# Optimization experiments

Measured on AMD Instinct MI355X. Metric: run time of the kernel, lower is better.

The kernel has to match this reference:

```python
import jax, jax.numpy as jnp
import numpy as np

T, D = 256, 256
N, F, DM, H1, H2 = T + D, 2048, 512, 128, 64
E_HALF = T * D            # edges with src < dst (track -> detection)
LAM, SLACK = 5.0, -0.2    # hardcoded in original forward
SINK_ITERS = 8


def setup_inputs() -> dict:
    key = jax.random.key(0)
    ks = jax.random.split(key, 16)
    x = jax.random.normal(ks[0], (N, F), jnp.float32)
    coords = jax.random.normal(ks[1], (N, 4), jnp.float32)
    # boxes in xyxy with positive extent for IoU
    c = jax.random.uniform(ks[2], (N, 2), jnp.float32) * 0.8
    wh = jax.random.uniform(ks[3], (N, 2), jnp.float32) * 0.2 + 0.01
    coords_original = jnp.concatenate([c, c + wh], axis=1)
    ground_truth = (jax.random.uniform(ks[4], (E_HALF,)) < 0.1).astype(jnp.float32)
    # full bipartite directed edges: first half track->det (src<dst), second half reversed
    t = jnp.arange(T, dtype=jnp.int32)
    d = jnp.arange(D, dtype=jnp.int32) + T
    src_h = jnp.repeat(t, D)
    dst_h = jnp.tile(d, T)
    edge_index = jnp.stack([jnp.concatenate([src_h, dst_h]),
                            jnp.concatenate([dst_h, src_h])])

    def w(k, shape, fan_in):
        return jax.random.normal(k, shape, jnp.float32) / np.sqrt(fan_in).astype(np.float32)

    params = dict(
        W_enc=w(ks[5], (F, DM), F), b_enc=jnp.zeros((DM,), jnp.float32),
        app_W1=w(ks[6], (2 * DM, H1), 2 * DM), app_b1=jnp.zeros((H1,), jnp.float32),
        app_w2=w(ks[7], (H1,), H1), app_b2=jnp.zeros((), jnp.float32),
        geo_W1=w(ks[8], (8, H2), 8), geo_b1=jnp.zeros((H2,), jnp.float32),
        geo_w2=w(ks[9], (H2,), H2), geo_b2=jnp.zeros((), jnp.float32),
        aff_w=w(ks[10], (2,), 2), aff_b=jnp.zeros((), jnp.float32),
        W_self=w(ks[11], (DM, DM), DM), W_nbr=w(ks[12], (DM, DM), DM),
        b_mp=jnp.zeros((DM,), jnp.float32),
        fin_w=w(ks[13], (2,), 2), fin_b=jnp.zeros((), jnp.float32),
    )
    return dict(x=x, coords=coords, coords_original=coords_original,
                ground_truth=ground_truth, edge_index=edge_index, **params)


def _box_iou(a, b):
    # a, b: [E, 4] xyxy boxes
    lt = jnp.maximum(a[:, :2], b[:, :2])
    rb = jnp.minimum(a[:, 2:], b[:, 2:])
    wh = jnp.clip(rb - lt, 0.0)
    inter = wh[:, 0] * wh[:, 1]
    area_a = (a[:, 2] - a[:, 0]) * (a[:, 3] - a[:, 1])
    area_b = (b[:, 2] - b[:, 0]) * (b[:, 3] - b[:, 1])
    return inter / (area_a + area_b - inter + 1e-6)


def _forward(x, coords, coords_original, edge_index,
             W_enc, b_enc, app_W1, app_b1, app_w2, app_b2,
             geo_W1, geo_b1, geo_w2, geo_b2, aff_w, aff_b,
             W_self, W_nbr, b_mp, fin_w, fin_b):
    src, dst = edge_index[0], edge_index[1]
    # EncoderCNN -> node embeddings [N, DM]
    h = jax.nn.relu(x @ W_enc + b_enc)
    hs, hd = h[src], h[dst]                       # per-edge gathers [E, DM]
    # appearance affinity MLP on concat embeddings -> scalar per edge
    x1 = jax.nn.sigmoid(jax.nn.relu(jnp.concatenate([hs, hd], 1) @ app_W1 + app_b1) @ app_w2 + app_b2)
    # geometric affinity MLP on concat coords -> scalar per edge
    geo = jnp.concatenate([coords[src], coords[dst]], 1)   # [E, 8]
    x2 = jax.nn.sigmoid(jax.nn.relu(geo @ geo_W1 + geo_b1) @ geo_w2 + geo_b2)
    iou = _box_iou(coords_original[src], coords_original[dst])   # [E]
    # combine -> edge weight (affinityNet)
    ew = jax.nn.sigmoid(jnp.stack([x1, x2], axis=-1) @ aff_w + aff_b)  # [E]
    # optimNet: weighted message passing -> updated node embeddings
    agg = jax.ops.segment_sum(ew[:, None] * (hs @ W_nbr), dst, num_segments=N)
    out = jax.nn.relu(h @ W_self + agg + b_mp)    # [N, DM]
    # edges with src < dst are exactly the first E_HALF by construction
    a, b = out[src[:E_HALF]], out[dst[:E_HALF]]
    na = jnp.clip(jnp.linalg.norm(a, axis=1), 1e-6)
    nb = jnp.clip(jnp.linalg.norm(b, axis=1), 1e-6)
    cos = jnp.sum(a * b, axis=1) / (na * nb)
    fin = jax.nn.sigmoid(jnp.stack([cos, iou[:E_HALF]], axis=-1) @ fin_w + fin_b)  # [E_HALF]
    # scatter-built cost matrix with slack row/column, Sinkhorn normalization
    sv = jnp.exp(jnp.float32(SLACK * LAM))
    M = jnp.zeros((T + 1, D + 1), jnp.float32)
    M = M.at[src[:E_HALF], dst[:E_HALF] - T].set(jnp.exp(fin * LAM))
    M = M.at[:, D].set(sv)
    M = M.at[T, :].set(sv)
    for _ in range(SINK_ITERS):
        M = M / jnp.sum(M, axis=1, keepdims=True)
        M = M / jnp.sum(M, axis=0, keepdims=True)
    return M[:T, :D].reshape(-1)   # [T*D]


def reference(x, coords, coords_original, ground_truth, edge_index,
              W_enc, b_enc, app_W1, app_b1, app_w2, app_b2,
              geo_W1, geo_b1, geo_w2, geo_b2, aff_w, aff_b,
              W_self, W_nbr, b_mp, fin_w, fin_b):
    normalized = _forward(x, coords, coords_original, edge_index,
                          W_enc, b_enc, app_W1, app_b1, app_w2, app_b2,
                          geo_W1, geo_b1, geo_w2, geo_b2, aff_w, aff_b,
                          W_self, W_nbr, b_mp, fin_w, fin_b)
    # post-Sinkhorn entries are strictly positive, so the !=0 filter is identity
    det_num = jnp.full((1,), D, jnp.int32)
    tracklet_num = jnp.full((1,), T, jnp.int32)
    return normalized, ground_truth, det_num, tracklet_num
```

## Files before the change

### kernel.cpp

```cpp
#include <hip/hip_runtime.h>
#include <hip/hip_fp16.h>
#include <math.h>

#define EH   65536
#define LAMF 5.0f
#define SVF  0.36787944117144233f

typedef __bf16 bf16x8 __attribute__((ext_vector_type(8)));
typedef float  f32x4  __attribute__((ext_vector_type(4)));
typedef _Float16 f16x2 __attribute__((ext_vector_type(2)));

__device__ __forceinline__ float sigmoidf_(float x) { return 1.0f / (1.0f + expf(-x)); }

__device__ __forceinline__ void cvt1(float v, ushort& h, ushort& l) {
    __bf16 bh = (__bf16)v;
    h = __builtin_bit_cast(ushort, bh);
    __bf16 bl = (__bf16)(v - (float)bh);
    l = __builtin_bit_cast(ushort, bl);
}

__device__ __forceinline__ f16x2 u2h(uint u) { return __builtin_bit_cast(f16x2, u); }

#define LSTR 40
template<int MODE>
__global__ __launch_bounds__(256) void gemm64(
    const float* __restrict__ Aa, const float* __restrict__ Ab,
    const float* __restrict__ B0, const float* __restrict__ B1,
    const float* __restrict__ B2,
    const float* __restrict__ HsC45, const float* __restrict__ bmp,
    float* __restrict__ C0, float* __restrict__ C1)
{
    __shared__ ushort As_hi[64*LSTR], As_lo[64*LSTR], Bs_hi[64*LSTR], Bs_lo[64*LSTR];
    const int tid = threadIdx.x;
    const int row0 = blockIdx.y * 64;

    const float* Ap = Aa; int lda, arow0 = row0, ak = 0;
    const float* Bp; int ldb, kb = 0, bcol0;
    float* Cp; int ldc, ccol0;
    int KS;

    if (MODE == 0) {
        KS = 256; lda = 2048; ak = blockIdx.z * 256;
        Bp = B0; ldb = 512; kb = blockIdx.z * 256; bcol0 = blockIdx.x * 64;
        Cp = C0 + blockIdx.z * 262144; ldc = 512; ccol0 = bcol0;
    } else if (MODE == 1) {
        KS = 512; lda = 512;
        int cb = blockIdx.x;
        if (cb < 8)       { Bp=B0; ldb=512; kb=0;   bcol0=cb*64;        Cp=C0; ldc=1024; ccol0=cb*64; }
        else if (cb < 16) { Bp=B1; ldb=512; kb=0;   bcol0=(cb-8)*64;    Cp=C0; ldc=1024; ccol0=512+(cb-8)*64; }
        else if (cb < 18) { Bp=B2; ldb=128; kb=0;   bcol0=(cb-16)*64;   Cp=C1; ldc=256;  ccol0=(cb-16)*64; }
        else              { Bp=B2; ldb=128; kb=512; bcol0=(cb-18)*64;   Cp=C1; ldc=256;  ccol0=128+(cb-18)*64; }
    } else {
        KS = 256; lda = 256;
        if (row0 < 256) { Ap = Aa; arow0 = row0;       kb = 256; }
        else            { Ap = Ab; arow0 = row0 - 256; kb = 0; }
        Bp = B0; ldb = 1024; bcol0 = blockIdx.x * 64;
        Cp = C0; ldc = 512; ccol0 = bcol0;
    }

    const int arow = tid >> 2, kq = (tid & 3) * 8;
    const int kr = (tid & 15) * 2, nc0 = (tid >> 4) * 4;
    const float* aptr = Ap + (size_t)(arow0 + arow) * lda + ak + kq;
    const float* bptr = Bp + (size_t)(kb + kr) * ldb + bcol0 + nc0;

    f32x4 acc[2][2] = {};
    const int lane = tid & 63, w = tid >> 6;
    const int qr = (w >> 1) * 32, qc = (w & 1) * 32;
    const int fr = lane & 15, kg = (lane >> 4) * 8;

    float4 pa0, pa1, pb0, pb1;
    pa0 = *(const float4*)aptr; pa1 = *(const float4*)(aptr + 4);
    pb0 = *(const float4*)bptr; pb1 = *(const float4*)(bptr + ldb);

    for (int k0 = 0; k0 < KS; k0 += 32) {
        {
            ushort4 h0, l0, h1, l1;
            cvt1(pa0.x,h0.x,l0.x); cvt1(pa0.y,h0.y,l0.y); cvt1(pa0.z,h0.z,l0.z); cvt1(pa0.w,h0.w,l0.w);
            cvt1(pa1.x,h1.x,l1.x); cvt1(pa1.y,h1.y,l1.y); cvt1(pa1.z,h1.z,l1.z); cvt1(pa1.w,h1.w,l1.w);
            *(ushort4*)&As_hi[arow*LSTR + kq]     = h0;
            *(ushort4*)&As_hi[arow*LSTR + kq + 4] = h1;
            *(ushort4*)&As_lo[arow*LSTR + kq]     = l0;
            *(ushort4*)&As_lo[arow*LSTR + kq + 4] = l1;
            float b0a[4] = {pb0.x, pb0.y, pb0.z, pb0.w};
            float b1a[4] = {pb1.x, pb1.y, pb1.z, pb1.w};
            #pragma unroll
            for (int j = 0; j < 4; ++j) {
                ushort ha, la, hb, lb;
                cvt1(b0a[j], ha, la); cvt1(b1a[j], hb, lb);
                *(uint*)&Bs_hi[(nc0+j)*LSTR + kr] = (uint)ha | ((uint)hb << 16);
                *(uint*)&Bs_lo[(nc0+j)*LSTR + kr] = (uint)la | ((uint)lb << 16);
            }
        }
        __syncthreads();
        if (k0 + 32 < KS) {
            pa0 = *(const float4*)(aptr + k0 + 32);
            pa1 = *(const float4*)(aptr + k0 + 36);
            const float* bp2 = bptr + (size_t)(k0 + 32) * ldb;
            pb0 = *(const float4*)bp2; pb1 = *(const float4*)(bp2 + ldb);
        }
        bf16x8 ah[2], al[2], bh[2], bl[2];
        #pragma unroll
        for (int m = 0; m < 2; ++m) {
            int r = (qr + m*16 + fr) * LSTR + kg;
            ah[m] = *(const bf16x8*)&As_hi[r];
            al[m] = *(const bf16x8*)&As_lo[r];
        }
        #pragma unroll
        for (int n = 0; n < 2; ++n) {
            int r = (qc + n*16 + fr) * LSTR + kg;
            bh[n] = *(const bf16x8*)&Bs_hi[r];
            bl[n] = *(const bf16x8*)&Bs_lo[r];
        }
        #pragma unroll
        for (int m = 0; m < 2; ++m)
            #pragma unroll
            for (int n = 0; n < 2; ++n) {
                acc[m][n] = __builtin_amdgcn_mfma_f32_16x16x32_bf16(ah[m], bh[n], acc[m][n], 0, 0, 0);
                acc[m][n] = __builtin_amdgcn_mfma_f32_16x16x32_bf16(ah[m], bl[n], acc[m][n], 0, 0, 0);
                acc[m][n] = __builtin_amdgcn_mfma_f32_16x16x32_bf16(al[m], bh[n], acc[m][n], 0, 0, 0);
            }
        __syncthreads();
    }

    const int rbase = (lane >> 4) * 4;
    #pragma unroll
    for (int m = 0; m < 2; ++m)
        #pragma unroll
        for (int n = 0; n < 2; ++n)
            #pragma unroll
            for (int r = 0; r < 4; ++r) {
                int gr = row0 + qr + m*16 + rbase + r;
                int gc = ccol0 + qc + n*16 + (lane & 15);
                float v = acc[m][n][r];
                if (MODE == 2) {
                    v += HsC45[(size_t)gr * 1024 + 512 + gc] + bmp[gc];
                    v = fmaxf(v, 0.f);
                }
                Cp[(size_t)gr * ldc + gc] = v;
            }
}

__global__ __launch_bounds__(256) void enc_reduce(const float* __restrict__ P,
    const float* __restrict__ bias, float* __restrict__ h)
{
    int e = (blockIdx.x * 256 + threadIdx.x) * 4;
    int col = e & 511;
    float4 s = *(const float4*)&P[e];
    #pragma unroll
    for (int z = 1; z < 8; ++z) {
        float4 v = *(const float4*)&P[e + z * 262144];
        s.x += v.x; s.y += v.y; s.z += v.z; s.w += v.w;
    }
    float4 b = *(const float4*)&bias[col];
    float4 o;
    o.x = fmaxf(s.x + b.x, 0.f);
    o.y = fmaxf(s.y + b.y, 0.f);
    o.z = fmaxf(s.z + b.z, 0.f);
    o.w = fmaxf(s.w + b.w, 0.f);
    *(float4*)&h[e] = o;
}

__global__ __launch_bounds__(256) void edge_geo_kernel(
    const float* __restrict__ C23, const float* __restrict__ coords,
    const float* __restrict__ geo_W1, const float* __restrict__ geo_b1,
    const float* __restrict__ app_b1, const float* __restrict__ app_w2,
    const float* __restrict__ app_b2, const float* __restrict__ geo_w2,
    const float* __restrict__ geo_b2, const float* __restrict__ aff_w,
    const float* __restrict__ aff_b, const float* __restrict__ co,
    const float* __restrict__ gt, float* __restrict__ outp,
    float* __restrict__ ewT0, float* __restrict__ ew2, float* __restrict__ iou1)
{
    __shared__ __align__(16) float sA[16][132], sB[16][132];
    __shared__ __align__(16) float sGA[16][68], sGB[16][68];
    __shared__ __align__(16) float sw2[128], sgw2[64];
    __shared__ float sgw[8][64], sgb[64], scs[16][4], scd[16][4];
    const int tid = threadIdx.x;
    const int half = blockIdx.z;
    const int t0 = blockIdx.y * 16, d0 = blockIdx.x * 16;
    const int sbase = half ? (256 + d0) : t0;
    const int dbase = half ? t0 : (256 + d0);

    if (half == 1) {
        int bid = blockIdx.y * 16 + blockIdx.x;
        if (tid < 64) {
            int o = bid * 256 + tid * 4;
            *(float4*)&outp[EH + o] = *(const float4*)&gt[o];
        }
        if (bid == 0 && tid == 64) {
            outp[2 * EH]     = 256.0f;
            outp[2 * EH + 1] = 256.0f;
        }
    }

    for (int i = tid; i < 16 * 32; i += 256) {
        int rr = i >> 5, c4 = (i & 31) << 2;
        float4 va = *(const float4*)&C23[(sbase + rr) * 256 + c4];
        sA[rr][c4] = va.x; sA[rr][c4+1] = va.y; sA[rr][c4+2] = va.z; sA[rr][c4+3] = va.w;
        float4 vb = *(const float4*)&C23[(dbase + rr) * 256 + 128 + c4];
        float4 b1 = *(const float4*)&app_b1[c4];
        sB[rr][c4] = vb.x + b1.x; sB[rr][c4+1] = vb.y + b1.y;
        sB[rr][c4+2] = vb.z + b1.z; sB[rr][c4+3] = vb.w + b1.w;
    }
    for (int i = tid; i < 512; i += 256) sgw[i >> 6][i & 63] = geo_W1[i];
    if (tid < 64) sgb[tid] = geo_b1[tid];
    else if (tid < 192) sw2[tid - 64] = app_w2[tid - 64];
    else sgw2[tid - 192] = geo_w2[tid - 192];
    if (tid < 64) scs[tid >> 2][tid & 3] = coords[(sbase + (tid >> 2)) * 4 + (tid & 3)];
    else if (tid < 128) { int i = tid - 64; scd[i >> 2][i & 3] = coords[(dbase + (i >> 2)) * 4 + (i & 3)]; }
    __syncthreads();
    for (int v = tid; v < 2048; v += 256) {
        int hh = v >> 10, rr = (v >> 6) & 15, j = v & 63;
        if (hh == 0) {
            sGA[rr][j] = scs[rr][0]*sgw[0][j] + scs[rr][1]*sgw[1][j]
                       + scs[rr][2]*sgw[2][j] + scs[rr][3]*sgw[3][j] + sgb[j];
        } else {
            sGB[rr][j] = scd[rr][0]*sgw[4][j] + scd[rr][1]*sgw[5][j]
                       + scd[rr][2]*sgw[6][j] + scd[rr][3]*sgw[7][j];
        }
    }
    __syncthreads();
    const int tx = tid & 15, ty = tid >> 4;
    const int si = half ? tx : ty;
    const int di = half ? ty : tx;
    float acc1 = 0.f;
    #pragma unroll
    for (int j4 = 0; j4 < 128; j4 += 4) {
        float4 a = *(const float4*)&sA[si][j4];
        float4 b = *(const float4*)&sB[di][j4];
        float4 wv = *(const float4*)&sw2[j4];
        acc1 += fmaxf(a.x + b.x, 0.f) * wv.x + fmaxf(a.y + b.y, 0.f) * wv.y
              + fmaxf(a.z + b.z, 0.f) * wv.z + fmaxf(a.w + b.w, 0.f) * wv.w;
    }
    float x1 = sigmoidf_(acc1 + app_b2[0]);
    float acc2 = 0.f;
    #pragma unroll
    for (int j4 = 0; j4 < 64; j4 += 4) {
        float4 a = *(const float4*)&sGA[si][j4];
        float4 b = *(const float4*)&sGB[di][j4];
        float4 wv = *(const float4*)&sgw2[j4];
        acc2 += fmaxf(a.x + b.x, 0.f) * wv.x + fmaxf(a.y + b.y, 0.f) * wv.y
              + fmaxf(a.z + b.z, 0.f) * wv.z + fmaxf(a.w + b.w, 0.f) * wv.w;
    }
    float x2 = sigmoidf_(acc2 + geo_b2[0]);
    float e = sigmoidf_(x1 * aff_w[0] + x2 * aff_w[1] + aff_b[0]);
    const int t = t0 + ty, d = d0 + tx;
    if (half) ew2[t * 256 + d] = e;
    else      ewT0[d * 256 + t] = e;
    if (half == 0) {
        float4 a = *(const float4*)&co[t * 4];
        float4 b = *(const float4*)&co[(256 + d) * 4];
        float ltx = fmaxf(a.x, b.x), lty = fmaxf(a.y, b.y);
        float rbx = fminf(a.z, b.z), rby = fminf(a.w, b.w);
        float w  = fmaxf(rbx - ltx, 0.f), hh = fmaxf(rby - lty, 0.f);
        float inter = w * hh;
        float areaA = (a.z - a.x) * (a.w - a.y);
        float areaB = (b.z - b.x) * (b.w - b.y);
        iou1[t * 256 + d] = inter / (areaA + areaB - inter + 1e-6f);
    }
}

__global__ __launch_bounds__(256) void gram32(const float* __restrict__ outm,
    const float* __restrict__ iou, const float* __restrict__ finw,
    const float* __restrict__ finb, __half* __restrict__ Mh)
{
    __shared__ ushort As_hi[32*LSTR], As_lo[32*LSTR], Bs_hi[32*LSTR], Bs_lo[32*LSTR];
    __shared__ float snA[32], snB[32];
    const int tid = threadIdx.x;
    const int t0 = blockIdx.y * 32, d0 = blockIdx.x * 32;
    const float* Asrc = outm;
    const float* Bsrc = outm + (size_t)256 * 512;

    const int arow = tid >> 3, kq = (tid & 7) * 4;
    const float* aptr = Asrc + (size_t)(t0 + arow) * 512 + kq;
    const float* bptr = Bsrc + (size_t)(d0 + arow) * 512 + kq;

    f32x4 acc = {};
    float ssA = 0.f, ssB = 0.f;
    const int lane = tid & 63, w = tid >> 6;
    const int qr = (w >> 1) * 16, qc = (w & 1) * 16;
    const int fr = lane & 15, kg = (lane >> 4) * 8;

    float4 pa = *(const float4*)aptr;
    float4 pb = *(const float4*)bptr;

    for (int k0 = 0; k0 < 512; k0 += 32) {
        ssA += pa.x*pa.x + pa.y*pa.y + pa.z*pa.z + pa.w*pa.w;
        ssB += pb.x*pb.x + pb.y*pb.y + pb.z*pb.z + pb.w*pb.w;
        {
            ushort4 h4, l4;
            cvt1(pa.x,h4.x,l4.x); cvt1(pa.y,h4.y,l4.y); cvt1(pa.z,h4.z,l4.z); cvt1(pa.w,h4.w,l4.w);
            *(ushort4*)&As_hi[arow*LSTR + kq] = h4;
            *(ushort4*)&As_lo[arow*LSTR + kq] = l4;
            cvt1(pb.x,h4.x,l4.x); cvt1(pb.y,h4.y,l4.y); cvt1(pb.z,h4.z,l4.z); cvt1(pb.w,h4.w,l4.w);
            *(ushort4*)&Bs_hi[arow*LSTR + kq] = h4;
            *(ushort4*)&Bs_lo[arow*LSTR + kq] = l4;
        }
        __syncthreads();
        if (k0 + 32 < 512) {
            pa = *(const float4*)(aptr + k0 + 32);
            pb = *(const float4*)(bptr + k0 + 32);
        }
        bf16x8 ah, al, bh, bl;
        {
            int r = (qr + fr) * LSTR + kg;
            ah = *(const bf16x8*)&As_hi[r]; al = *(const bf16x8*)&As_lo[r];
        }
        {
            int r = (qc + fr) * LSTR + kg;
            bh = *(const bf16x8*)&Bs_hi[r]; bl = *(const bf16x8*)&Bs_lo[r];
        }
        acc = __builtin_amdgcn_mfma_f32_16x16x32_bf16(ah, bh, acc, 0, 0, 0);
        acc = __builtin_amdgcn_mfma_f32_16x16x32_bf16(ah, bl, acc, 0, 0, 0);
        acc = __builtin_amdgcn_mfma_f32_16x16x32_bf16(al, bh, acc, 0, 0, 0);
        __syncthreads();
    }
    ssA += __shfl_xor(ssA, 1); ssA += __shfl_xor(ssA, 2); ssA += __shfl_xor(ssA, 4);
    ssB += __shfl_xor(ssB, 1); ssB += __shfl_xor(ssB, 2); ssB += __shfl_xor(ssB, 4);
    if ((tid & 7) == 0) { snA[arow] = ssA; snB[arow] = ssB; }
    __syncthreads();
    const float fw0 = finw[0], fw1 = finw[1], fb = finb[0];
    const int rbase = (lane >> 4) * 4, lc = qc + (lane & 15);
    #pragma unroll
    for (int r = 0; r < 4; ++r) {
        int lr = qr + rbase + r;
        float na = fmaxf(sqrtf(snA[lr]), 1e-6f);
        float nb = fmaxf(sqrtf(snB[lc]), 1e-6f);
        int t = t0 + lr, d = d0 + lc;
        float cosv = acc[r] / (na * nb);
        float fin = sigmoidf_(cosv * fw0 + iou[t * 256 + d] * fw1 + fb);
        Mh[t * 256 + d] = __float2half(expf(fin * LAMF));
    }
}

__global__ __launch_bounds__(1024, 4) void sinkhorn4(const __half* __restrict__ Mh,
    float* __restrict__ gr, float* __restrict__ gc)
{
    __shared__ float r_f[256], c_f[256], red[16];
    __shared__ __half r_h[256], c_h[256];
    const int tid = threadIdx.x;
    const int row = tid >> 2, sub4 = tid & 3;
    const int cg = tid >> 5, sub32 = tid & 31;

    const uint4* gm = (const uint4*)Mh;
    uint4 mr[8];
    #pragma unroll
    for (int j = 0; j < 8; ++j) mr[j] = gm[row * 32 + sub4 * 8 + j];
    uint4 mca[4], mcb[4];
    #pragma unroll
    for (int p = 0; p < 4; ++p) {
        int rp = 2 * sub32 + 64 * p;
        mca[p] = gm[rp * 32 + cg];
        mcb[p] = gm[(rp + 1) * 32 + cg];
    }
    if (tid < 256) { c_f[tid] = 1.0f; c_h[tid] = __float2half(1.0f); }
    if (tid == 0) red[1] = 1.0f / SVF;
    __syncthreads();

    const int b4 = (sub32 >> 4) & 1, b3 = (sub32 >> 3) & 1, b2 = (sub32 >> 2) & 1;

    for (int it = 0; it < 8; ++it) {
        float c256 = 1.0f / (SVF * red[1]);
        float a0 = 0.f, a1 = 0.f, a2 = 0.f, a3 = 0.f;
        {
            uint4 cu[4];
            #pragma unroll
            for (int j = 0; j < 4; ++j) cu[j] = *(const uint4*)&c_h[sub4 * 64 + j * 8];
            #pragma unroll
            for (int j = 0; j < 4; ++j) {
                a0 = __builtin_amdgcn_fdot2(u2h(mr[j].x), u2h(cu[j].x), a0, false);
                a1 = __builtin_amdgcn_fdot2(u2h(mr[j].y), u2h(cu[j].y), a1, false);
                a2 = __builtin_amdgcn_fdot2(u2h(mr[j].z), u2h(cu[j].z), a2, false);
                a3 = __builtin_amdgcn_fdot2(u2h(mr[j].w), u2h(cu[j].w), a3, false);
            }
            #pragma unroll
            for (int j = 0; j < 4; ++j) cu[j] = *(const uint4*)&c_h[sub4 * 64 + 32 + j * 8];
            #pragma unroll
            for (int j = 0; j < 4; ++j) {
                a0 = __builtin_amdgcn_fdot2(u2h(mr[4+j].x), u2h(cu[j].x), a0, false);
                a1 = __builtin_amdgcn_fdot2(u2h(mr[4+j].y), u2h(cu[j].y), a1, false);
                a2 = __builtin_amdgcn_fdot2(u2h(mr[4+j].z), u2h(cu[j].z), a2, false);
                a3 = __builtin_amdgcn_fdot2(u2h(mr[4+j].w), u2h(cu[j].w), a3, false);
            }
        }
        float acc = (a0 + a1) + (a2 + a3);
        acc += __shfl_xor(acc, 1); acc += __shfl_xor(acc, 2);
        if (tid < 64) {
            float s = c_f[tid] + c_f[tid + 64] + c_f[tid + 128] + c_f[tid + 192];
            #pragma unroll
            for (int o = 32; o; o >>= 1) s += __shfl_down(s, o);
            if (tid == 0) red[0] = s + c256;
        }
        if (sub4 == 0) {
            float v = 1.0f / (acc + SVF * c256);
            r_f[row] = v; r_h[row] = __float2half(v);
        }
        __syncthreads();

        float r256 = 1.0f / (SVF * red[0]);
        float b[8] = {0.f,0.f,0.f,0.f,0.f,0.f,0.f,0.f};
        #pragma unroll
        for (int p = 0; p < 4; ++p) {
            f16x2 rp = u2h(*(const uint*)&r_h[2 * sub32 + 64 * p]);
            uint lo, hi;
            lo = __builtin_amdgcn_perm(mcb[p].x, mca[p].x, 0x05040100);
            hi = __builtin_amdgcn_perm(mcb[p].x, mca[p].x, 0x07060302);
            b[0] = __builtin_amdgcn_fdot2(u2h(lo), rp, b[0], false);
            b[1] = __builtin_amdgcn_fdot2(u2h(hi), rp, b[1], false);
            lo = __builtin_amdgcn_perm(mcb[p].y, mca[p].y, 0x05040100);
            hi = __builtin_amdgcn_perm(mcb[p].y, mca[p].y, 0x07060302);
            b[2] = __builtin_amdgcn_fdot2(u2h(lo), rp, b[2], false);
            b[3] = __builtin_amdgcn_fdot2(u2h(hi), rp, b[3], false);
            lo = __builtin_amdgcn_perm(mcb[p].z, mca[p].z, 0x05040100);
            hi = __builtin_amdgcn_perm(mcb[p].z, mca[p].z, 0x07060302);
            b[4] = __builtin_amdgcn_fdot2(u2h(lo), rp, b[4], false);
            b[5] = __builtin_amdgcn_fdot2(u2h(hi), rp, b[5], false);
            lo = __builtin_amdgcn_perm(mcb[p].w, mca[p].w, 0x05040100);
            hi = __builtin_amdgcn_perm(mcb[p].w, mca[p].w, 0x07060302);
            b[6] = __builtin_amdgcn_fdot2(u2h(lo), rp, b[6], false);
            b[7] = __builtin_amdgcn_fdot2(u2h(hi), rp, b[7], false);
        }
        float t0v, t1v, t2v, t3v;
        t0v = b4 ? b[0] : b[4]; t1v = b4 ? b[1] : b[5];
        t2v = b4 ? b[2] : b[6]; t3v = b4 ? b[3] : b[7];
        t0v = __shfl_xor(t0v, 16); t1v = __shfl_xor(t1v, 16);
        t2v = __shfl_xor(t2v, 16); t3v = __shfl_xor(t3v, 16);
        float k0 = (b4 ? b[4] : b[0]) + t0v;
        float k1 = (b4 ? b[5] : b[1]) + t1v;
        float k2 = (b4 ? b[6] : b[2]) + t2v;
        float k3 = (b4 ? b[7] : b[3]) + t3v;
        float u0 = b3 ? k0 : k2, u1 = b3 ? k1 : k3;
        u0 = __shfl_xor(u0, 8); u1 = __shfl_xor(u1, 8);
        float m0 = (b3 ? k2 : k0) + u0;
        float m1 = (b3 ? k3 : k1) + u1;
        float w0 = b2 ? m0 : m1;
        w0 = __shfl_xor(w0, 4);
        float s = (b2 ? m1 : m0) + w0;
        s += __shfl_xor(s, 1); s += __shfl_xor(s, 2);
        if (tid < 64) {
            float s2 = r_f[tid] + r_f[tid + 64] + r_f[tid + 128] + r_f[tid + 192];
            #pragma unroll
            for (int o = 32; o; o >>= 1) s2 += __shfl_down(s2, o);
            if (tid == 0) red[1] = s2 + r256;
        }
        if ((sub32 & 3) == 0) {
            int col = cg * 8 + b4 * 4 + b3 * 2 + b2;
            float v = 1.0f / (s + SVF * r256);
            c_f[col] = v; c_h[col] = __float2half(v);
        }
        __syncthreads();
    }
    if (tid < 256) { gr[tid] = r_f[tid]; gc[tid] = c_f[tid]; }
}

__global__ __launch_bounds__(256) void final_kernel(const __half* __restrict__ Mh,
    const float* __restrict__ r, const float* __restrict__ c,
    float* __restrict__ out)
{
    const int bid = blockIdx.x, tid = threadIdx.x;
    int k = bid * 256 + tid;
    out[k] = __half2float(Mh[k]) * r[bid] * c[tid];
}

extern "C" void kernel_launch(void* const* d_in, const int* in_sizes, int n_in,
                              void* d_out, int out_size, void* d_ws, size_t ws_size,
                              hipStream_t stream)
{
    const float* x       = (const float*)d_in[0];
    const float* coords  = (const float*)d_in[1];
    const float* co      = (const float*)d_in[2];
    const float* gt      = (const float*)d_in[3];
    const float* W_enc   = (const float*)d_in[5];
    const float* b_enc   = (const float*)d_in[6];
    const float* app_W1  = (const float*)d_in[7];
    const float* app_b1  = (const float*)d_in[8];
    const float* app_w2  = (const float*)d_in[9];
    const float* app_b2  = (const float*)d_in[10];
    const float* geo_W1  = (const float*)d_in[11];
    const float* geo_b1  = (const float*)d_in[12];
    const float* geo_w2  = (const float*)d_in[13];
    const float* geo_b2  = (const float*)d_in[14];
    const float* aff_w   = (const float*)d_in[15];
    const float* aff_b   = (const float*)d_in[16];
    const float* W_self  = (const float*)d_in[17];
    const float* W_nbr   = (const float*)d_in[18];
    const float* b_mp    = (const float*)d_in[19];
    const float* fin_w   = (const float*)d_in[20];
    const float* fin_b   = (const float*)d_in[21];
    float* out = (float*)d_out;

    char* W = (char*)d_ws;
    float*  P     = (float*)(W + 0);
    float*  h     = (float*)(W + 8388608);
    float*  C45   = (float*)(W + 0);
    float*  C23   = (float*)(W + 2097152);
    float*  ewT0  = (float*)(W + 2621440);
    float*  ew2   = (float*)(W + 2883584);
    float*  iou1  = (float*)(W + 3145728);
    __half* Mh    = (__half*)(W + 3407872);
    float*  grv   = (float*)(W + 3538944);
    float*  gcv   = (float*)(W + 3543040);
    float*  outm  = (float*)(W + 3670016);

    gemm64<0><<<dim3(8, 8, 8), 256, 0, stream>>>(x, nullptr, W_enc, nullptr, nullptr,
        nullptr, nullptr, P, nullptr);
    enc_reduce<<<256, 256, 0, stream>>>(P, b_enc, h);
    gemm64<1><<<dim3(20, 8), 256, 0, stream>>>(h, nullptr, W_nbr, W_self, app_W1,
        nullptr, nullptr, C45, C23);
    edge_geo_kernel<<<dim3(16, 16, 2), 256, 0, stream>>>(C23, coords, geo_W1, geo_b1,
        app_b1, app_w2, app_b2, geo_w2, geo_b2, aff_w, aff_b, co, gt, out,
        ewT0, ew2, iou1);
    gemm64<2><<<dim3(8, 8), 256, 0, stream>>>(ew2, ewT0, C45, nullptr, nullptr,
        C45, b_mp, outm, nullptr);
    gram32<<<dim3(8, 8), 256, 0, stream>>>(outm, iou1, fin_w, fin_b, Mh);
    sinkhorn4<<<1, 1024, 0, stream>>>(Mh, grv, gcv);
    final_kernel<<<256, 256, 0, stream>>>(Mh, grv, gcv, out);
}
```

Baseline: 83.81 us.

## Fuse final scaling into Sinkhorn kernel and halve GEMM2 row tile

The separate final_kernel launch is removed: the single-block Sinkhorn kernel now holds the whole matrix in registers with 512 threads, each owning 128 half values, and writes the scaled output itself. This drops one launch and the global round trip of the row and column scale vectors. The column operand permutes are hoisted out of the iteration loop. Separately, gemm64 MODE 2 uses 32-row tiles so its grid doubles to 128 blocks for more parallelism. The trade-off is much higher register pressure per thread in Sinkhorn and the final write being done by a single block.

```diff
diff --git a/kernel.cpp b/kernel.cpp
--- a/kernel.cpp
+++ b/kernel.cpp
@@ -20,6 +20,10 @@
 }
 
 __device__ __forceinline__ f16x2 u2h(uint u) { return __builtin_bit_cast(f16x2, u); }
+__device__ __forceinline__ float2 h2f2u(uint u) {
+    __half2 h = __builtin_bit_cast(__half2, u);
+    return __half22float2(h);
+}
 
 #define LSTR 40
 template<int MODE>
@@ -30,9 +34,10 @@
     const float* __restrict__ HsC45, const float* __restrict__ bmp,
     float* __restrict__ C0, float* __restrict__ C1)
 {
+    constexpr int MT = (MODE == 2) ? 1 : 2;
     __shared__ ushort As_hi[64*LSTR], As_lo[64*LSTR], Bs_hi[64*LSTR], Bs_lo[64*LSTR];
     const int tid = threadIdx.x;
-    const int row0 = blockIdx.y * 64;
+    const int row0 = blockIdx.y * (MT * 32);
 
     const float* Ap = Aa; int lda, arow0 = row0, ak = 0;
     const float* Bp; int ldb, kb = 0, bcol0;
@@ -58,29 +63,34 @@
         Cp = C0; ldc = 512; ccol0 = bcol0;
     }
 
-    const int arow = tid >> 2, kq = (tid & 3) * 8;
+    const int arow = (MT == 2) ? (tid >> 2) : (tid >> 3);
+    const int kq   = (MT == 2) ? ((tid & 3) * 8) : ((tid & 7) * 4);
     const int kr = (tid & 15) * 2, nc0 = (tid >> 4) * 4;
     const float* aptr = Ap + (size_t)(arow0 + arow) * lda + ak + kq;
     const float* bptr = Bp + (size_t)(kb + kr) * ldb + bcol0 + nc0;
 
-    f32x4 acc[2][2] = {};
+    f32x4 acc[MT][2] = {};
     const int lane = tid & 63, w = tid >> 6;
-    const int qr = (w >> 1) * 32, qc = (w & 1) * 32;
+    const int qr = (w >> 1) * (MT * 16), qc = (w & 1) * 32;
     const int fr = lane & 15, kg = (lane >> 4) * 8;
 
     float4 pa0, pa1, pb0, pb1;
-    pa0 = *(const float4*)aptr; pa1 = *(const float4*)(aptr + 4);
+    pa0 = *(const float4*)aptr;
+    if (MT == 2) pa1 = *(const float4*)(aptr + 4);
     pb0 = *(const float4*)bptr; pb1 = *(const float4*)(bptr + ldb);
 
     for (int k0 = 0; k0 < KS; k0 += 32) {
         {
-            ushort4 h0, l0, h1, l1;
+            ushort4 h0, l0;
             cvt1(pa0.x,h0.x,l0.x); cvt1(pa0.y,h0.y,l0.y); cvt1(pa0.z,h0.z,l0.z); cvt1(pa0.w,h0.w,l0.w);
-            cvt1(pa1.x,h1.x,l1.x); cvt1(pa1.y,h1.y,l1.y); cvt1(pa1.z,h1.z,l1.z); cvt1(pa1.w,h1.w,l1.w);
-            *(ushort4*)&As_hi[arow*LSTR + kq]     = h0;
-            *(ushort4*)&As_hi[arow*LSTR + kq + 4] = h1;
-            *(ushort4*)&As_lo[arow*LSTR + kq]     = l0;
-            *(ushort4*)&As_lo[arow*LSTR + kq + 4] = l1;
+            *(ushort4*)&As_hi[arow*LSTR + kq] = h0;
+            *(ushort4*)&As_lo[arow*LSTR + kq] = l0;
+            if (MT == 2) {
+                ushort4 h1, l1;
+                cvt1(pa1.x,h1.x,l1.x); cvt1(pa1.y,h1.y,l1.y); cvt1(pa1.z,h1.z,l1.z); cvt1(pa1.w,h1.w,l1.w);
+                *(ushort4*)&As_hi[arow*LSTR + kq + 4] = h1;
+                *(ushort4*)&As_lo[arow*LSTR + kq + 4] = l1;
+            }
             float b0a[4] = {pb0.x, pb0.y, pb0.z, pb0.w};
             float b1a[4] = {pb1.x, pb1.y, pb1.z, pb1.w};
             #pragma unroll
@@ -94,13 +104,13 @@
         __syncthreads();
         if (k0 + 32 < KS) {
             pa0 = *(const float4*)(aptr + k0 + 32);
-            pa1 = *(const float4*)(aptr + k0 + 36);
+            if (MT == 2) pa1 = *(const float4*)(aptr + k0 + 36);
             const float* bp2 = bptr + (size_t)(k0 + 32) * ldb;
             pb0 = *(const float4*)bp2; pb1 = *(const float4*)(bp2 + ldb);
         }
-        bf16x8 ah[2], al[2], bh[2], bl[2];
+        bf16x8 ah[MT], al[MT], bh[2], bl[2];
         #pragma unroll
-        for (int m = 0; m < 2; ++m) {
+        for (int m = 0; m < MT; ++m) {
             int r = (qr + m*16 + fr) * LSTR + kg;
             ah[m] = *(const bf16x8*)&As_hi[r];
             al[m] = *(const bf16x8*)&As_lo[r];
@@ -112,7 +122,7 @@
             bl[n] = *(const bf16x8*)&Bs_lo[r];
         }
         #pragma unroll
-        for (int m = 0; m < 2; ++m)
+        for (int m = 0; m < MT; ++m)
             #pragma unroll
             for (int n = 0; n < 2; ++n) {
                 acc[m][n] = __builtin_amdgcn_mfma_f32_16x16x32_bf16(ah[m], bh[n], acc[m][n], 0, 0, 0);
@@ -124,7 +134,7 @@
 
     const int rbase = (lane >> 4) * 4;
     #pragma unroll
-    for (int m = 0; m < 2; ++m)
+    for (int m = 0; m < MT; ++m)
         #pragma unroll
         for (int n = 0; n < 2; ++n)
             #pragma unroll
@@ -332,133 +342,124 @@
     }
 }
 
-__global__ __launch_bounds__(1024, 4) void sinkhorn4(const __half* __restrict__ Mh,
-    float* __restrict__ gr, float* __restrict__ gc)
+__global__ __launch_bounds__(512, 2) void sinkhorn5(const __half* __restrict__ Mh,
+    float* __restrict__ out)
 {
-    __shared__ float r_f[256], c_f[256], red[16];
+    __shared__ float r_f[256], c_f[256], red[8];
     __shared__ __half r_h[256], c_h[256];
     const int tid = threadIdx.x;
-    const int row = tid >> 2, sub4 = tid & 3;
-    const int cg = tid >> 5, sub32 = tid & 31;
+    const int row = tid >> 1, hf = tid & 1;
+    const int cg = tid >> 4, s16 = tid & 15;
 
     const uint4* gm = (const uint4*)Mh;
-    uint4 mr[8];
-    #pragma unroll
-    for (int j = 0; j < 8; ++j) mr[j] = gm[row * 32 + sub4 * 8 + j];
-    uint4 mca[4], mcb[4];
-    #pragma unroll
-    for (int p = 0; p < 4; ++p) {
-        int rp = 2 * sub32 + 64 * p;
-        mca[p] = gm[rp * 32 + cg];
-        mcb[p] = gm[(rp + 1) * 32 + cg];
+    uint4 mr[16];
+    #pragma unroll
+    for (int j = 0; j < 16; ++j) mr[j] = gm[row * 32 + hf * 16 + j];
+    uint mc[64];
+    #pragma unroll
+    for (int p = 0; p < 8; ++p) {
+        int rA = 2 * s16 + 32 * p;
+        uint4 aa = gm[rA * 32 + cg];
+        uint4 bb = gm[(rA + 1) * 32 + cg];
+        mc[p*8+0] = __builtin_amdgcn_perm(bb.x, aa.x, 0x05040100);
+        mc[p*8+1] = __builtin_amdgcn_perm(bb.x, aa.x, 0x07060302);
+        mc[p*8+2] = __builtin_amdgcn_perm(bb.y, aa.y, 0x05040100);
+        mc[p*8+3] = __builtin_amdgcn_perm(bb.y, aa.y, 0x07060302);
+        mc[p*8+4] = __builtin_amdgcn_perm(bb.z, aa.z, 0x05040100);
+        mc[p*8+5] = __builtin_amdgcn_perm(bb.z, aa.z, 0x07060302);
+        mc[p*8+6] = __builtin_amdgcn_perm(bb.w, aa.w, 0x05040100);
+        mc[p*8+7] = __builtin_amdgcn_perm(bb.w, aa.w, 0x07060302);
     }
     if (tid < 256) { c_f[tid] = 1.0f; c_h[tid] = __float2half(1.0f); }
     if (tid == 0) red[1] = 1.0f / SVF;
     __syncthreads();
 
-    const int b4 = (sub32 >> 4) & 1, b3 = (sub32 >> 3) & 1, b2 = (sub32 >> 2) & 1;
+    const int s8 = s16 & 8, s4 = s16 & 4, s2 = s16 & 2;
+    const int mycol = cg * 8 + (s8 ? 4 : 0) + (s4 ? 2 : 0) + (s2 ? 1 : 0);
 
     for (int it = 0; it < 8; ++it) {
         float c256 = 1.0f / (SVF * red[1]);
         float a0 = 0.f, a1 = 0.f, a2 = 0.f, a3 = 0.f;
-        {
-            uint4 cu[4];
-            #pragma unroll
-            for (int j = 0; j < 4; ++j) cu[j] = *(const uint4*)&c_h[sub4 * 64 + j * 8];
-            #pragma unroll
-            for (int j = 0; j < 4; ++j) {
-                a0 = __builtin_amdgcn_fdot2(u2h(mr[j].x), u2h(cu[j].x), a0, false);
-                a1 = __builtin_amdgcn_fdot2(u2h(mr[j].y), u2h(cu[j].y), a1, false);
-                a2 = __builtin_amdgcn_fdot2(u2h(mr[j].z), u2h(cu[j].z), a2, false);
-                a3 = __builtin_amdgcn_fdot2(u2h(mr[j].w), u2h(cu[j].w), a3, false);
-            }
-            #pragma unroll
-            for (int j = 0; j < 4; ++j) cu[j] = *(const uint4*)&c_h[sub4 * 64 + 32 + j * 8];
-            #pragma unroll
-            for (int j = 0; j < 4; ++j) {
-                a0 = __builtin_amdgcn_fdot2(u2h(mr[4+j].x), u2h(cu[j].x), a0, false);
-                a1 = __builtin_amdgcn_fdot2(u2h(mr[4+j].y), u2h(cu[j].y), a1, false);
-                a2 = __builtin_amdgcn_fdot2(u2h(mr[4+j].z), u2h(cu[j].z), a2, false);
-                a3 = __builtin_amdgcn_fdot2(u2h(mr[4+j].w), u2h(cu[j].w), a3, false);
-            }
+        #pragma unroll
+        for (int j = 0; j < 16; ++j) {
+            uint4 cu = *(const uint4*)&c_h[hf * 128 + j * 8];
+            a0 = __builtin_amdgcn_fdot2(u2h(mr[j].x), u2h(cu.x), a0, false);
+            a1 = __builtin_amdgcn_fdot2(u2h(mr[j].y), u2h(cu.y), a1, false);
+            a2 = __builtin_amdgcn_fdot2(u2h(mr[j].z), u2h(cu.z), a2, false);
+            a3 = __builtin_amdgcn_fdot2(u2h(mr[j].w), u2h(cu.w), a3, false);
         }
         float acc = (a0 + a1) + (a2 + a3);
-        acc += __shfl_xor(acc, 1); acc += __shfl_xor(acc, 2);
+        acc += __shfl_xor(acc, 1);
         if (tid < 64) {
             float s = c_f[tid] + c_f[tid + 64] + c_f[tid + 128] + c_f[tid + 192];
             #pragma unroll
             for (int o = 32; o; o >>= 1) s += __shfl_down(s, o);
             if (tid == 0) red[0] = s + c256;
         }
-        if (sub4 == 0) {
+        if (hf == 0) {
             float v = 1.0f / (acc + SVF * c256);
             r_f[row] = v; r_h[row] = __float2half(v);
         }
         __syncthreads();
 
         float r256 = 1.0f / (SVF * red[0]);
-        float b[8] = {0.f,0.f,0.f,0.f,0.f,0.f,0.f,0.f};
+        float b0=0.f,b1=0.f,b2=0.f,b3=0.f,b4=0.f,b5=0.f,b6=0.f,b7=0.f;
         #pragma unroll
-        for (int p = 0; p < 4; ++p) {
-            f16x2 rp = u2h(*(const uint*)&r_h[2 * sub32 + 64 * p]);
-            uint lo, hi;
-            lo = __builtin_amdgcn_perm(mcb[p].x, mca[p].x, 0x05040100);
-            hi = __builtin_amdgcn_perm(mcb[p].x, mca[p].x, 0x07060302);
-            b[0] = __builtin_amdgcn_fdot2(u2h(lo), rp, b[0], false);
-            b[1] = __builtin_amdgcn_fdot2(u2h(hi), rp, b[1], false);
-            lo = __builtin_amdgcn_perm(mcb[p].y, mca[p].y, 0x05040100);
-            hi = __builtin_amdgcn_perm(mcb[p].y, mca[p].y, 0x07060302);
-            b[2] = __builtin_amdgcn_fdot2(u2h(lo), rp, b[2], false);
-            b[3] = __builtin_amdgcn_fdot2(u2h(hi), rp, b[3], false);
-            lo = __builtin_amdgcn_perm(mcb[p].z, mca[p].z, 0x05040100);
-            hi = __builtin_amdgcn_perm(mcb[p].z, mca[p].z, 0x07060302);
-            b[4] = __builtin_amdgcn_fdot2(u2h(lo), rp, b[4], false);
-            b[5] = __builtin_amdgcn_fdot2(u2h(hi), rp, b[5], false);
-            lo = __builtin_amdgcn_perm(mcb[p].w, mca[p].w, 0x05040100);
-            hi = __builtin_amdgcn_perm(mcb[p].w, mca[p].w, 0x07060302);
-            b[6] = __builtin_amdgcn_fdot2(u2h(lo), rp, b[6], false);
-            b[7] = __builtin_amdgcn_fdot2(u2h(hi), rp, b[7], false);
-        }
-        float t0v, t1v, t2v, t3v;
-        t0v = b4 ? b[0] : b[4]; t1v = b4 ? b[1] : b[5];
-        t2v = b4 ? b[2] : b[6]; t3v = b4 ? b[3] : b[7];
-        t0v = __shfl_xor(t0v, 16); t1v = __shfl_xor(t1v, 16);
-        t2v = __shfl_xor(t2v, 16); t3v = __shfl_xor(t3v, 16);
-        float k0 = (b4 ? b[4] : b[0]) + t0v;
-        float k1 = (b4 ? b[5] : b[1]) + t1v;
-        float k2 = (b4 ? b[6] : b[2]) + t2v;
-        float k3 = (b4 ? b[7] : b[3]) + t3v;
-        float u0 = b3 ? k0 : k2, u1 = b3 ? k1 : k3;
-        u0 = __shfl_xor(u0, 8); u1 = __shfl_xor(u1, 8);
-        float m0 = (b3 ? k2 : k0) + u0;
-        float m1 = (b3 ? k3 : k1) + u1;
-        float w0 = b2 ? m0 : m1;
-        w0 = __shfl_xor(w0, 4);
-        float s = (b2 ? m1 : m0) + w0;
-        s += __shfl_xor(s, 1); s += __shfl_xor(s, 2);
+        for (int p = 0; p < 8; ++p) {
+            f16x2 rp = u2h(*(const uint*)&r_h[2 * s16 + 32 * p]);
+            b0 = __builtin_amdgcn_fdot2(u2h(mc[p*8+0]), rp, b0, false);
+            b1 = __builtin_amdgcn_fdot2(u2h(mc[p*8+1]), rp, b1, false);
+            b2 = __builtin_amdgcn_fdot2(u2h(mc[p*8+2]), rp, b2, false);
+            b3 = __builtin_amdgcn_fdot2(u2h(mc[p*8+3]), rp, b3, false);
+            b4 = __builtin_amdgcn_fdot2(u2h(mc[p*8+4]), rp, b4, false);
+            b5 = __builtin_amdgcn_fdot2(u2h(mc[p*8+5]), rp, b5, false);
+            b6 = __builtin_amdgcn_fdot2(u2h(mc[p*8+6]), rp, b6, false);
+            b7 = __builtin_amdgcn_fdot2(u2h(mc[p*8+7]), rp, b7, false);
+        }
+        float t0 = s8 ? b0 : b4, t1 = s8 ? b1 : b5, t2 = s8 ? b2 : b6, t3 = s8 ? b3 : b7;
+        t0 = __shfl_xor(t0, 8); t1 = __shfl_xor(t1, 8);
+        t2 = __shfl_xor(t2, 8); t3 = __shfl_xor(t3, 8);
+        float k0 = (s8 ? b4 : b0) + t0;
+        float k1 = (s8 ? b5 : b1) + t1;
+        float k2 = (s8 ? b6 : b2) + t2;
+        float k3 = (s8 ? b7 : b3) + t3;
+        float u0 = s4 ? k0 : k2, u1 = s4 ? k1 : k3;
+        u0 = __shfl_xor(u0, 4); u1 = __shfl_xor(u1, 4);
+        float m0 = (s4 ? k2 : k0) + u0;
+        float m1 = (s4 ? k3 : k1) + u1;
+        float w0 = s2 ? m0 : m1;
+        w0 = __shfl_xor(w0, 2);
+        float s = (s2 ? m1 : m0) + w0;
+        s += __shfl_xor(s, 1);
         if (tid < 64) {
-            float s2 = r_f[tid] + r_f[tid + 64] + r_f[tid + 128] + r_f[tid + 192];
+            float s2v = r_f[tid] + r_f[tid + 64] + r_f[tid + 128] + r_f[tid + 192];
             #pragma unroll
-            for (int o = 32; o; o >>= 1) s2 += __shfl_down(s2, o);
-            if (tid == 0) red[1] = s2 + r256;
-        }
-        if ((sub32 & 3) == 0) {
-            int col = cg * 8 + b4 * 4 + b3 * 2 + b2;
+            for (int o = 32; o; o >>= 1) s2v += __shfl_down(s2v, o);
+            if (tid == 0) red[1] = s2v + r256;
+        }
+        if ((s16 & 1) == 0) {
             float v = 1.0f / (s + SVF * r256);
-            c_f[col] = v; c_h[col] = __float2half(v);
+            c_f[mycol] = v; c_h[mycol] = __float2half(v);
         }
         __syncthreads();
     }
-    if (tid < 256) { gr[tid] = r_f[tid]; gc[tid] = c_f[tid]; }
-}
-
-__global__ __launch_bounds__(256) void final_kernel(const __half* __restrict__ Mh,
-    const float* __restrict__ r, const float* __restrict__ c,
-    float* __restrict__ out)
-{
-    const int bid = blockIdx.x, tid = threadIdx.x;
-    int k = bid * 256 + tid;
-    out[k] = __half2float(Mh[k]) * r[bid] * c[tid];
+
+    float rv = r_f[row];
+    #pragma unroll
+    for (int j = 0; j < 16; ++j) {
+        int cb = hf * 128 + j * 8;
+        float4 ca = *(const float4*)&c_f[cb];
+        float4 cbv = *(const float4*)&c_f[cb + 4];
+        float2 f0 = h2f2u(mr[j].x), f1 = h2f2u(mr[j].y);
+        float2 f2 = h2f2u(mr[j].z), f3 = h2f2u(mr[j].w);
+        float4 o0, o1;
+        o0.x = f0.x * rv * ca.x;  o0.y = f0.y * rv * ca.y;
+        o0.z = f1.x * rv * ca.z;  o0.w = f1.y * rv * ca.w;
+        o1.x = f2.x * rv * cbv.x; o1.y = f2.y * rv * cbv.y;
+        o1.z = f3.x * rv * cbv.z; o1.w = f3.y * rv * cbv.w;
+        *(float4*)&out[row * 256 + cb]     = o0;
+        *(float4*)&out[row * 256 + cb + 4] = o1;
+    }
 }
 
 extern "C" void kernel_launch(void* const* d_in, const int* in_sizes, int n_in,
@@ -497,8 +498,6 @@
     float*  ew2   = (float*)(W + 2883584);
     float*  iou1  = (float*)(W + 3145728);
     __half* Mh    = (__half*)(W + 3407872);
-    float*  grv   = (float*)(W + 3538944);
-    float*  gcv   = (float*)(W + 3543040);
     float*  outm  = (float*)(W + 3670016);
 
     gemm64<0><<<dim3(8, 8, 8), 256, 0, stream>>>(x, nullptr, W_enc, nullptr, nullptr,
@@ -509,9 +508,8 @@
     edge_geo_kernel<<<dim3(16, 16, 2), 256, 0, stream>>>(C23, coords, geo_W1, geo_b1,
         app_b1, app_w2, app_b2, geo_w2, geo_b2, aff_w, aff_b, co, gt, out,
         ewT0, ew2, iou1);
-    gemm64<2><<<dim3(8, 8), 256, 0, stream>>>(ew2, ewT0, C45, nullptr, nullptr,
+    gemm64<2><<<dim3(8, 16), 256, 0, stream>>>(ew2, ewT0, C45, nullptr, nullptr,
         C45, b_mp, outm, nullptr);
     gram32<<<dim3(8, 8), 256, 0, stream>>>(outm, iou1, fin_w, fin_b, Mh);
-    sinkhorn4<<<1, 1024, 0, stream>>>(Mh, grv, gcv);
-    final_kernel<<<256, 256, 0, stream>>>(Mh, grv, gcv, out);
-}
+    sinkhorn5<<<1, 512, 0, stream>>>(Mh, out);
+}
```

Measured after the change: 89.58 us. 6.9% more time.

## Fuse split-K encoder reduction into next GEMM's A-tile load, halve split count

Applied to the files above, without the earlier changes.

The encoder GEMM now uses split-K of 4 with K=512 per slice instead of 8 slices of 256. The separate enc_reduce kernel is removed: the MODE 1 GEMM loads the four partial slices directly, sums them, adds the bias and applies ReLU while staging its A tile. This drops one launch and the write/read of the reduced h buffer. The trade-off is fewer blocks in the encoder GEMM, and every MODE 1 column block repeats the 4-way partial reads and reduction. The workspace is relaid out so the outputs no longer overlap the partial buffer.

```diff
diff --git a/kernel.cpp b/kernel.cpp
--- a/kernel.cpp
+++ b/kernel.cpp
@@ -20,13 +20,17 @@
 }
 
 __device__ __forceinline__ f16x2 u2h(uint u) { return __builtin_bit_cast(f16x2, u); }
+__device__ __forceinline__ float2 h2f2u(uint u) {
+    __half2 h = __builtin_bit_cast(__half2, u);
+    return __half22float2(h);
+}
 
 #define LSTR 40
 template<int MODE>
 __global__ __launch_bounds__(256) void gemm64(
     const float* __restrict__ Aa, const float* __restrict__ Ab,
     const float* __restrict__ B0, const float* __restrict__ B1,
-    const float* __restrict__ B2,
+    const float* __restrict__ B2, const float* __restrict__ bias,
     const float* __restrict__ HsC45, const float* __restrict__ bmp,
     float* __restrict__ C0, float* __restrict__ C1)
 {
@@ -34,14 +38,14 @@
     const int tid = threadIdx.x;
     const int row0 = blockIdx.y * 64;
 
-    const float* Ap = Aa; int lda, arow0 = row0, ak = 0;
+    const float* Ap = Aa; int lda = 0, arow0 = row0, ak = 0;
     const float* Bp; int ldb, kb = 0, bcol0;
     float* Cp; int ldc, ccol0;
     int KS;
 
     if (MODE == 0) {
-        KS = 256; lda = 2048; ak = blockIdx.z * 256;
-        Bp = B0; ldb = 512; kb = blockIdx.z * 256; bcol0 = blockIdx.x * 64;
+        KS = 512; lda = 2048; ak = blockIdx.z * 512;
+        Bp = B0; ldb = 512; kb = blockIdx.z * 512; bcol0 = blockIdx.x * 64;
         Cp = C0 + blockIdx.z * 262144; ldc = 512; ccol0 = bcol0;
     } else if (MODE == 1) {
         KS = 512; lda = 512;
@@ -60,8 +64,9 @@
 
     const int arow = tid >> 2, kq = (tid & 3) * 8;
     const int kr = (tid & 15) * 2, nc0 = (tid >> 4) * 4;
-    const float* aptr = Ap + (size_t)(arow0 + arow) * lda + ak + kq;
-    const float* bptr = Bp + (size_t)(kb + kr) * ldb + bcol0 + nc0;
+    const float* aptr  = Ap + (size_t)(arow0 + arow) * lda + ak + kq;
+    const float* aptrP = Aa + (size_t)(arow0 + arow) * 512 + kq;
+    const float* bptr  = Bp + (size_t)(kb + kr) * ldb + bcol0 + nc0;
 
     f32x4 acc[2][2] = {};
     const int lane = tid & 63, w = tid >> 6;
@@ -69,14 +74,36 @@
     const int fr = lane & 15, kg = (lane >> 4) * 8;
 
     float4 pa0, pa1, pb0, pb1;
-    pa0 = *(const float4*)aptr; pa1 = *(const float4*)(aptr + 4);
+    float4 pz0[4], pz1[4];
+    if constexpr (MODE == 1) {
+        #pragma unroll
+        for (int z = 0; z < 4; ++z) {
+            pz0[z] = *(const float4*)(aptrP + z * 262144);
+            pz1[z] = *(const float4*)(aptrP + z * 262144 + 4);
+        }
+    } else {
+        pa0 = *(const float4*)aptr; pa1 = *(const float4*)(aptr + 4);
+    }
     pb0 = *(const float4*)bptr; pb1 = *(const float4*)(bptr + ldb);
 
     for (int k0 = 0; k0 < KS; k0 += 32) {
+        float4 sa0, sa1;
+        if constexpr (MODE == 1) {
+            float4 b0v = *(const float4*)&bias[k0 + kq];
+            float4 b1v = *(const float4*)&bias[k0 + kq + 4];
+            sa0.x = fmaxf(pz0[0].x + pz0[1].x + pz0[2].x + pz0[3].x + b0v.x, 0.f);
+            sa0.y = fmaxf(pz0[0].y + pz0[1].y + pz0[2].y + pz0[3].y + b0v.y, 0.f);
+            sa0.z = fmaxf(pz0[0].z + pz0[1].z + pz0[2].z + pz0[3].z + b0v.z, 0.f);
+            sa0.w = fmaxf(pz0[0].w + pz0[1].w + pz0[2].w + pz0[3].w + b0v.w, 0.f);
+            sa1.x = fmaxf(pz1[0].x + pz1[1].x + pz1[2].x + pz1[3].x + b1v.x, 0.f);
+            sa1.y = fmaxf(pz1[0].y + pz1[1].y + pz1[2].y + pz1[3].y + b1v.y, 0.f);
+            sa1.z = fmaxf(pz1[0].z + pz1[1].z + pz1[2].z + pz1[3].z + b1v.z, 0.f);
+            sa1.w = fmaxf(pz1[0].w + pz1[1].w + pz1[2].w + pz1[3].w + b1v.w, 0.f);
+        } else { sa0 = pa0; sa1 = pa1; }
         {
             ushort4 h0, l0, h1, l1;
-            cvt1(pa0.x,h0.x,l0.x); cvt1(pa0.y,h0.y,l0.y); cvt1(pa0.z,h0.z,l0.z); cvt1(pa0.w,h0.w,l0.w);
-            cvt1(pa1.x,h1.x,l1.x); cvt1(pa1.y,h1.y,l1.y); cvt1(pa1.z,h1.z,l1.z); cvt1(pa1.w,h1.w,l1.w);
+            cvt1(sa0.x,h0.x,l0.x); cvt1(sa0.y,h0.y,l0.y); cvt1(sa0.z,h0.z,l0.z); cvt1(sa0.w,h0.w,l0.w);
+            cvt1(sa1.x,h1.x,l1.x); cvt1(sa1.y,h1.y,l1.y); cvt1(sa1.z,h1.z,l1.z); cvt1(sa1.w,h1.w,l1.w);
             *(ushort4*)&As_hi[arow*LSTR + kq]     = h0;
             *(ushort4*)&As_hi[arow*LSTR + kq + 4] = h1;
             *(ushort4*)&As_lo[arow*LSTR + kq]     = l0;
@@ -93,8 +120,16 @@
         }
         __syncthreads();
         if (k0 + 32 < KS) {
-            pa0 = *(const float4*)(aptr + k0 + 32);
-            pa1 = *(const float4*)(aptr + k0 + 36);
+            if constexpr (MODE == 1) {
+                #pragma unroll
+                for (int z = 0; z < 4; ++z) {
+                    pz0[z] = *(const float4*)(aptrP + z * 262144 + k0 + 32);
+                    pz1[z] = *(const float4*)(aptrP + z * 262144 + k0 + 36);
+                }
+            } else {
+                pa0 = *(const float4*)(aptr + k0 + 32);
+                pa1 = *(const float4*)(aptr + k0 + 36);
+            }
             const float* bp2 = bptr + (size_t)(k0 + 32) * ldb;
             pb0 = *(const float4*)bp2; pb1 = *(const float4*)(bp2 + ldb);
         }
@@ -138,26 +173,6 @@
                 }
                 Cp[(size_t)gr * ldc + gc] = v;
             }
-}
-
-__global__ __launch_bounds__(256) void enc_reduce(const float* __restrict__ P,
-    const float* __restrict__ bias, float* __restrict__ h)
-{
-    int e = (blockIdx.x * 256 + threadIdx.x) * 4;
-    int col = e & 511;
-    float4 s = *(const float4*)&P[e];
-    #pragma unroll
-    for (int z = 1; z < 8; ++z) {
-        float4 v = *(const float4*)&P[e + z * 262144];
-        s.x += v.x; s.y += v.y; s.z += v.z; s.w += v.w;
-    }
-    float4 b = *(const float4*)&bias[col];
-    float4 o;
-    o.x = fmaxf(s.x + b.x, 0.f);
-    o.y = fmaxf(s.y + b.y, 0.f);
-    o.z = fmaxf(s.z + b.z, 0.f);
-    o.w = fmaxf(s.w + b.w, 0.f);
-    *(float4*)&h[e] = o;
 }
 
 __global__ __launch_bounds__(256) void edge_geo_kernel(
@@ -490,27 +505,25 @@
 
     char* W = (char*)d_ws;
     float*  P     = (float*)(W + 0);
-    float*  h     = (float*)(W + 8388608);
-    float*  C45   = (float*)(W + 0);
-    float*  C23   = (float*)(W + 2097152);
-    float*  ewT0  = (float*)(W + 2621440);
-    float*  ew2   = (float*)(W + 2883584);
-    float*  iou1  = (float*)(W + 3145728);
-    __half* Mh    = (__half*)(W + 3407872);
-    float*  grv   = (float*)(W + 3538944);
-    float*  gcv   = (float*)(W + 3543040);
-    float*  outm  = (float*)(W + 3670016);
-
-    gemm64<0><<<dim3(8, 8, 8), 256, 0, stream>>>(x, nullptr, W_enc, nullptr, nullptr,
-        nullptr, nullptr, P, nullptr);
-    enc_reduce<<<256, 256, 0, stream>>>(P, b_enc, h);
-    gemm64<1><<<dim3(20, 8), 256, 0, stream>>>(h, nullptr, W_nbr, W_self, app_W1,
-        nullptr, nullptr, C45, C23);
+    float*  C45   = (float*)(W + 4194304);
+    float*  C23   = (float*)(W + 6291456);
+    float*  ewT0  = (float*)(W + 6815744);
+    float*  ew2   = (float*)(W + 7077888);
+    float*  iou1  = (float*)(W + 7340032);
+    __half* Mh    = (__half*)(W + 7596288);
+    float*  grv   = (float*)(W + 7729152);
+    float*  gcv   = (float*)(W + 7733248);
+    float*  outm  = (float*)(W + 7737344);
+
+    gemm64<0><<<dim3(8, 8, 4), 256, 0, stream>>>(x, nullptr, W_enc, nullptr, nullptr,
+        nullptr, nullptr, nullptr, P, nullptr);
+    gemm64<1><<<dim3(20, 8), 256, 0, stream>>>(P, nullptr, W_nbr, W_self, app_W1,
+        b_enc, nullptr, nullptr, C45, C23);
     edge_geo_kernel<<<dim3(16, 16, 2), 256, 0, stream>>>(C23, coords, geo_W1, geo_b1,
         app_b1, app_w2, app_b2, geo_w2, geo_b2, aff_w, aff_b, co, gt, out,
         ewT0, ew2, iou1);
     gemm64<2><<<dim3(8, 8), 256, 0, stream>>>(ew2, ewT0, C45, nullptr, nullptr,
-        C45, b_mp, outm, nullptr);
+        nullptr, C45, b_mp, outm, nullptr);
     gram32<<<dim3(8, 8), 256, 0, stream>>>(outm, iou1, fin_w, fin_b, Mh);
     sinkhorn4<<<1, 1024, 0, stream>>>(Mh, grv, gcv);
     final_kernel<<<256, 256, 0, stream>>>(Mh, grv, gcv, out);
```

New measurement: 92.14 us. 1.1x slower.
